# Optimization experiments

Measured on AMD Instinct MI355X. Metric: run time of the kernel, lower is better.

## Reference

```python
import jax, jax.numpy as jnp
import numpy as np

N = 100000
E = 1600000
C_IN = 128
C_OUT = 128


def setup_inputs() -> dict:
    key = jax.random.key(0)
    k1, k2, k3 = jax.random.split(key, 3)
    x = jax.random.normal(k1, (N, C_IN), dtype=jnp.float32)
    edge_index = jax.random.randint(k2, (2, E), 0, N, dtype=jnp.int64)
    # Linear(in, out, bias=False).weight has shape [out, in]
    W = jax.random.normal(k3, (C_OUT, C_IN), dtype=jnp.float32) * (1.0 / np.sqrt(C_IN))
    return {"x": x, "edge_index": edge_index, "W": W}


def reference(x, edge_index, W):
    n_nodes = x.shape[0]
    row, col = edge_index[0], edge_index[1]
    # degree counts only out-edges of row (matches torch `degree(edge_index, N)`)
    deg = jax.ops.segment_sum(jnp.ones((row.shape[0],), dtype=x.dtype), row,
                              num_segments=n_nodes)
    # D_tilde = D + I  ->  normalization n = (deg + 1)^(-1/2)
    inv_sqrt = jax.lax.rsqrt(deg + 1.0)  # [N]
    xs = x * inv_sqrt[:, None]
    # x <- (A + I) x : gather sources (col), scatter-add to destinations (row),
    # plus identity (self) contribution
    agg = jax.ops.segment_sum(xs[col], row, num_segments=n_nodes) + xs
    out = agg * inv_sqrt[:, None]
    # x <- x W^T
    return jnp.matmul(out, W.T)
```

## Files before the change

kernel.cpp:

```cpp
#include <hip/hip_runtime.h>
#include <hip/hip_fp16.h>
#include <math.h>

#define C 128
#define BSHIFT 9
#define BWIDTH 512
#define NBMAX 256
#define COLBITS 17
#define P2CHUNK 4096
#define P3CAP 10240
#define CAP 9216
#define APITCH 136

typedef _Float16 v8hf __attribute__((ext_vector_type(8)));
typedef float v4f __attribute__((ext_vector_type(4)));

__global__ __launch_bounds__(256) void init_wconv_kernel(int* __restrict__ gcur, int NB,
                                                         const float4* __restrict__ W4,
                                                         __half2* __restrict__ Wh2,
                                                         int total4) {
    int t = threadIdx.x;
    if (blockIdx.x == 0) {
        if (t < NB) gcur[t] = t * CAP;
    } else {
        int i = (blockIdx.x - 1) * 256 + t;
        if (i < total4) {
            float4 v = W4[i];
            Wh2[i * 2]     = __floats2half2_rn(v.x, v.y);
            Wh2[i * 2 + 1] = __floats2half2_rn(v.z, v.w);
        }
    }
}

__global__ __launch_bounds__(256) void p2_scatter_kernel(const int* __restrict__ rowI,
                                                         const int* __restrict__ colI,
                                                         int* __restrict__ gcur,
                                                         unsigned* __restrict__ ebuf, int E) {
    __shared__ int cnt[NBMAX];
    __shared__ int sc[NBMAX];
    __shared__ int delta[NBMAX];
    __shared__ unsigned sorted[P2CHUNK];
    __shared__ unsigned char bkt[P2CHUNK];
    const int t = threadIdx.x;
    cnt[t] = 0;
    __syncthreads();
    const int e0 = blockIdx.x * P2CHUNK;
    int ranks[16];
#pragma unroll
    for (int k = 0; k < 16; ++k) {
        int e = e0 + k * 256 + t;
        if (e < E) ranks[k] = atomicAdd(&cnt[rowI[e] >> BSHIFT], 1);
    }
    __syncthreads();
    sc[t] = cnt[t];
    __syncthreads();
    for (int o = 1; o < 256; o <<= 1) {
        int v = (t >= o) ? sc[t - o] : 0;
        __syncthreads();
        sc[t] += v;
        __syncthreads();
    }
    {
        int c = cnt[t];
        int ls = sc[t] - c;
        int gb = c ? atomicAdd(&gcur[t], c) : 0;
        delta[t] = gb - ls;
        sc[t] = ls;
    }
    __syncthreads();
#pragma unroll
    for (int k = 0; k < 16; ++k) {
        int e = e0 + k * 256 + t;
        if (e < E) {
            int r = rowI[e];
            unsigned cc = (unsigned)colI[e];
            int b = r >> BSHIFT;
            int lp = sc[b] + ranks[k];
            sorted[lp] = ((unsigned)(r & (BWIDTH - 1)) << COLBITS) | cc;
            bkt[lp] = (unsigned char)b;
        }
    }
    __syncthreads();
    int total = E - e0; if (total > P2CHUNK) total = P2CHUNK;
#pragma unroll
    for (int k = 0; k < 16; ++k) {
        int i = k * 256 + t;
        if (i < total) ebuf[delta[bkt[i]] + i] = sorted[i];
    }
}

__global__ __launch_bounds__(512) void p3_place_kernel(const unsigned* __restrict__ ebuf,
                                                       const int* __restrict__ gcur,
                                                       int* __restrict__ offs_start,
                                                       int* __restrict__ offs_end,
                                                       float* __restrict__ inv,
                                                       int* __restrict__ csr,
                                                       const float4* __restrict__ x4,
                                                       __half2* __restrict__ xsh2, int N) {
    __shared__ int cnt[BWIDTH];
    __shared__ int sc[BWIDTH];
    __shared__ float invS[BWIDTH];
    __shared__ int sortedCol[P3CAP];
    const int b = blockIdx.x;
    const int t = threadIdx.x;
    const int rowBase = b << BSHIFT;
    const int eS = b * CAP;
    const int eE = gcur[b];

    cnt[t] = 0;
    __syncthreads();
    for (int j = eS + t; j < eE; j += 512)
        atomicAdd(&cnt[ebuf[j] >> COLBITS], 1);
    __syncthreads();
    sc[t] = cnt[t];
    __syncthreads();
    for (int o = 1; o < 512; o <<= 1) {
        int v = (t >= o) ? sc[t - o] : 0;
        __syncthreads();
        sc[t] += v;
        __syncthreads();
    }
    int node = rowBase + t;
    int myCnt = cnt[t];
    float iv = rsqrtf((float)myCnt + 1.0f);
    invS[t] = iv;
    if (node < N) {
        offs_start[node] = eS + sc[t] - myCnt;
        offs_end[node]   = eS + sc[t];
        inv[node] = iv;
    }
    __syncthreads();
    cnt[t] = sc[t] - myCnt;
    __syncthreads();
    for (int j = eS + t; j < eE; j += 512) {
        unsigned rc = ebuf[j];
        int slot = atomicAdd(&cnt[rc >> COLBITS], 1);
        int col = (int)(rc & ((1u << COLBITS) - 1));
        if (slot < P3CAP) sortedCol[slot] = col;
        else csr[eS + slot] = col;
    }
    __syncthreads();
    int total = eE - eS; if (total > P3CAP) total = P3CAP;
    for (int i = t; i < total; i += 512)
        csr[eS + i] = sortedCol[i];

    int rows = N - rowBase; if (rows > BWIDTH) rows = BWIDTH;
    int limit = rows * 32;
    const float4* xr = x4 + (size_t)rowBase * 32;
    __half2* xd = xsh2 + (size_t)rowBase * 64;
    for (int i = t; i < limit; i += 512) {
        int row = i >> 5, ch = i & 31;
        float sI = invS[row];
        float4 v = xr[(size_t)row * 32 + ch];
        xd[(size_t)row * 64 + ch * 2]     = __floats2half2_rn(v.x * sI, v.y * sI);
        xd[(size_t)row * 64 + ch * 2 + 1] = __floats2half2_rn(v.z * sI, v.w * sI);
    }
}

#define ACC4(vv)                                                   \
    {                                                              \
        const __half2* p_ = (const __half2*)&(vv);                 \
        _Pragma("unroll")                                          \
        for (int q = 0; q < 4; ++q) {                              \
            float2 f_ = __half22float2(p_[q]);                     \
            a[2 * q] += f_.x; a[2 * q + 1] += f_.y;                \
        }                                                          \
    }

__global__ __launch_bounds__(256) void gather_mm_kernel(const float4* __restrict__ xsh4,
                                                        const int* __restrict__ offs_start,
                                                        const int* __restrict__ offs_end,
                                                        const int* __restrict__ csr,
                                                        const float* __restrict__ inv,
                                                        const _Float16* __restrict__ Wh,
                                                        float* __restrict__ out, int N) {
    __shared__ _Float16 agg[16][APITCH];
    const int tid = threadIdx.x;
    const int base = blockIdx.x * 16;
    const int r = tid >> 4;
    const int c16 = tid & 15;
    const int node = base + r;

    float a[8] = {0, 0, 0, 0, 0, 0, 0, 0};
    if (node < N) {
        int s = offs_start[node];
        int e = offs_end[node];
        {
            float4 h = xsh4[(size_t)node * 16 + c16];
            const __half2* p = (const __half2*)&h;
#pragma unroll
            for (int q = 0; q < 4; ++q) {
                float2 f = __half22float2(p[q]);
                a[2 * q] = f.x; a[2 * q + 1] = f.y;
            }
        }
        int j = s;
        for (; j + 4 <= e; j += 4) {
            int c0 = csr[j], c1 = csr[j + 1], c2 = csr[j + 2], c3 = csr[j + 3];
            float4 v0 = xsh4[(size_t)c0 * 16 + c16];
            float4 v1 = xsh4[(size_t)c1 * 16 + c16];
            float4 v2 = xsh4[(size_t)c2 * 16 + c16];
            float4 v3 = xsh4[(size_t)c3 * 16 + c16];
            ACC4(v0) ACC4(v1) ACC4(v2) ACC4(v3)
        }
        for (; j < e; ++j) {
            int c = csr[j];
            float4 v = xsh4[(size_t)c * 16 + c16];
            ACC4(v)
        }
        float invn = inv[node];
#pragma unroll
        for (int q = 0; q < 8; ++q) a[q] *= invn;
    }
    {
        __half2 hh[4];
#pragma unroll
        for (int q = 0; q < 4; ++q) hh[q] = __floats2half2_rn(a[2 * q], a[2 * q + 1]);
        *(float4*)&agg[r][c16 * 8] = *(const float4*)hh;
    }
    __syncthreads();

    const int wave = tid >> 6;
    const int lane = tid & 63;
    const int rr = lane & 15;
    const int kg = lane >> 4;

    v8hf av[4];
#pragma unroll
    for (int kk = 0; kk < 4; ++kk)
        av[kk] = *(const v8hf*)&agg[rr][kg * 8 + kk * 32];

#pragma unroll
    for (int ti = 0; ti < 2; ++ti) {
        const int t = wave * 2 + ti;
        v4f acc = {0.0f, 0.0f, 0.0f, 0.0f};
        const v8hf* bp = (const v8hf*)(Wh + (size_t)(t * 16 + rr) * C + kg * 8);
#pragma unroll
        for (int kk = 0; kk < 4; ++kk)
            acc = __builtin_amdgcn_mfma_f32_16x16x32_f16(av[kk], bp[kk * 4], acc, 0, 0, 0);
#pragma unroll
        for (int reg = 0; reg < 4; ++reg) {
            int orow = base + kg * 4 + reg;
            if (orow < N) out[(size_t)orow * C + t * 16 + rr] = acc[reg];
        }
    }
}

extern "C" void kernel_launch(void* const* d_in, const int* in_sizes, int n_in,
                              void* d_out, int out_size, void* d_ws, size_t ws_size,
                              hipStream_t stream) {
    const float* x  = (const float*)d_in[0];
    const int*   ei = (const int*)d_in[1];
    const float* W  = (const float*)d_in[2];
    float* out = (float*)d_out;

    const int N = in_sizes[0] / C;
    const int E = in_sizes[1] / 2;
    const int* rowI = ei;
    const int* colI = ei + E;

    const int NB = (N + BWIDTH - 1) / BWIDTH;

    char* ws = (char*)d_ws;
    size_t off = 0;
    auto carve = [&](size_t bytes) -> void* {
        off = (off + 255) & ~(size_t)255;
        void* p = ws + off;
        off += bytes;
        return p;
    };
    int*      gcur       = (int*)carve((size_t)NBMAX * 4);
    int*      offs_start = (int*)carve((size_t)N * 4);
    int*      offs_end   = (int*)carve((size_t)N * 4);
    float*    inv        = (float*)carve((size_t)N * 4);
    int*      csr        = (int*)carve((size_t)NB * CAP * 4);
    __half2*  xsh        = (__half2*)carve((size_t)N * C * 2);
    unsigned* ebuf       = (unsigned*)carve((size_t)NB * CAP * 4);
    __half2*  Wh         = (__half2*)carve((size_t)C * C * 2);

    int wtotal4 = C * C / 4;
    init_wconv_kernel<<<1 + (wtotal4 + 255) / 256, 256, 0, stream>>>(
        gcur, NB, (const float4*)W, Wh, wtotal4);

    int nChunks = (E + P2CHUNK - 1) / P2CHUNK;
    p2_scatter_kernel<<<nChunks, 256, 0, stream>>>(rowI, colI, gcur, ebuf, E);
    p3_place_kernel<<<NB, 512, 0, stream>>>(ebuf, gcur, offs_start, offs_end, inv, csr,
                                            (const float4*)x, xsh, N);

    gather_mm_kernel<<<(N + 15) / 16, 256, 0, stream>>>((const float4*)xsh, offs_start,
                                                        offs_end, csr, inv,
                                                        (const _Float16*)Wh, out, N);
}
```

Baseline: 131.7 us.

## Move fp16 conversion of x into scatter kernel and apply source norm in gather

The fp32-to-fp16 conversion of x moves from the place kernel, which runs on only about 196 blocks, into the scatter kernel, which has many more blocks, so the conversion gets more parallelism. Because the degree is not yet known at that point, the source normalisation moves into the gather loop. There it becomes an extra per-edge load of inv[col] folded in with an FMA. The cost is an additional random 4-byte gather per edge in the gather kernel.

```diff
diff --git a/kernel.cpp b/kernel.cpp
--- a/kernel.cpp
+++ b/kernel.cpp
@@ -35,7 +35,9 @@
 __global__ __launch_bounds__(256) void p2_scatter_kernel(const int* __restrict__ rowI,
                                                          const int* __restrict__ colI,
                                                          int* __restrict__ gcur,
-                                                         unsigned* __restrict__ ebuf, int E) {
+                                                         unsigned* __restrict__ ebuf, int E,
+                                                         const float4* __restrict__ x4,
+                                                         __half2* __restrict__ xh2, int N) {
     __shared__ int cnt[NBMAX];
     __shared__ int sc[NBMAX];
     __shared__ int delta[NBMAX];
@@ -87,6 +89,13 @@
         int i = k * 256 + t;
         if (i < total) ebuf[delta[bkt[i]] + i] = sorted[i];
     }
+
+    int totalX4 = N * 32;
+    for (int i = blockIdx.x * 256 + t; i < totalX4; i += gridDim.x * 256) {
+        float4 v = x4[i];
+        xh2[i * 2]     = __floats2half2_rn(v.x, v.y);
+        xh2[i * 2 + 1] = __floats2half2_rn(v.z, v.w);
+    }
 }
 
 __global__ __launch_bounds__(512) void p3_place_kernel(const unsigned* __restrict__ ebuf,
@@ -94,12 +103,9 @@
                                                        int* __restrict__ offs_start,
                                                        int* __restrict__ offs_end,
                                                        float* __restrict__ inv,
-                                                       int* __restrict__ csr,
-                                                       const float4* __restrict__ x4,
-                                                       __half2* __restrict__ xsh2, int N) {
+                                                       int* __restrict__ csr, int N) {
     __shared__ int cnt[BWIDTH];
     __shared__ int sc[BWIDTH];
-    __shared__ float invS[BWIDTH];
     __shared__ int sortedCol[P3CAP];
     const int b = blockIdx.x;
     const int t = threadIdx.x;
@@ -122,12 +128,10 @@
     }
     int node = rowBase + t;
     int myCnt = cnt[t];
-    float iv = rsqrtf((float)myCnt + 1.0f);
-    invS[t] = iv;
     if (node < N) {
         offs_start[node] = eS + sc[t] - myCnt;
         offs_end[node]   = eS + sc[t];
-        inv[node] = iv;
+        inv[node] = rsqrtf((float)myCnt + 1.0f);
     }
     __syncthreads();
     cnt[t] = sc[t] - myCnt;
@@ -143,31 +147,20 @@
     int total = eE - eS; if (total > P3CAP) total = P3CAP;
     for (int i = t; i < total; i += 512)
         csr[eS + i] = sortedCol[i];
-
-    int rows = N - rowBase; if (rows > BWIDTH) rows = BWIDTH;
-    int limit = rows * 32;
-    const float4* xr = x4 + (size_t)rowBase * 32;
-    __half2* xd = xsh2 + (size_t)rowBase * 64;
-    for (int i = t; i < limit; i += 512) {
-        int row = i >> 5, ch = i & 31;
-        float sI = invS[row];
-        float4 v = xr[(size_t)row * 32 + ch];
-        xd[(size_t)row * 64 + ch * 2]     = __floats2half2_rn(v.x * sI, v.y * sI);
-        xd[(size_t)row * 64 + ch * 2 + 1] = __floats2half2_rn(v.z * sI, v.w * sI);
-    }
-}
-
-#define ACC4(vv)                                                   \
+}
+
+#define ACC4F(vv, sI)                                              \
     {                                                              \
         const __half2* p_ = (const __half2*)&(vv);                 \
         _Pragma("unroll")                                          \
         for (int q = 0; q < 4; ++q) {                              \
             float2 f_ = __half22float2(p_[q]);                     \
-            a[2 * q] += f_.x; a[2 * q + 1] += f_.y;                \
+            a[2 * q]     = fmaf(f_.x, (sI), a[2 * q]);             \
+            a[2 * q + 1] = fmaf(f_.y, (sI), a[2 * q + 1]);         \
         }                                                          \
     }
 
-__global__ __launch_bounds__(256) void gather_mm_kernel(const float4* __restrict__ xsh4,
+__global__ __launch_bounds__(256) void gather_mm_kernel(const float4* __restrict__ xh4,
                                                         const int* __restrict__ offs_start,
                                                         const int* __restrict__ offs_end,
                                                         const int* __restrict__ csr,
@@ -182,33 +175,31 @@
     const int node = base + r;
 
     float a[8] = {0, 0, 0, 0, 0, 0, 0, 0};
+    float invn = 0.0f;
     if (node < N) {
         int s = offs_start[node];
         int e = offs_end[node];
+        invn = inv[node];
         {
-            float4 h = xsh4[(size_t)node * 16 + c16];
-            const __half2* p = (const __half2*)&h;
-#pragma unroll
-            for (int q = 0; q < 4; ++q) {
-                float2 f = __half22float2(p[q]);
-                a[2 * q] = f.x; a[2 * q + 1] = f.y;
-            }
+            float4 h = xh4[(size_t)node * 16 + c16];
+            ACC4F(h, invn)
         }
         int j = s;
         for (; j + 4 <= e; j += 4) {
             int c0 = csr[j], c1 = csr[j + 1], c2 = csr[j + 2], c3 = csr[j + 3];
-            float4 v0 = xsh4[(size_t)c0 * 16 + c16];
-            float4 v1 = xsh4[(size_t)c1 * 16 + c16];
-            float4 v2 = xsh4[(size_t)c2 * 16 + c16];
-            float4 v3 = xsh4[(size_t)c3 * 16 + c16];
-            ACC4(v0) ACC4(v1) ACC4(v2) ACC4(v3)
+            float i0 = inv[c0], i1 = inv[c1], i2 = inv[c2], i3 = inv[c3];
+            float4 v0 = xh4[(size_t)c0 * 16 + c16];
+            float4 v1 = xh4[(size_t)c1 * 16 + c16];
+            float4 v2 = xh4[(size_t)c2 * 16 + c16];
+            float4 v3 = xh4[(size_t)c3 * 16 + c16];
+            ACC4F(v0, i0) ACC4F(v1, i1) ACC4F(v2, i2) ACC4F(v3, i3)
         }
         for (; j < e; ++j) {
             int c = csr[j];
-            float4 v = xsh4[(size_t)c * 16 + c16];
-            ACC4(v)
-        }
-        float invn = inv[node];
+            float ic = inv[c];
+            float4 v = xh4[(size_t)c * 16 + c16];
+            ACC4F(v, ic)
+        }
 #pragma unroll
         for (int q = 0; q < 8; ++q) a[q] *= invn;
     }
@@ -274,7 +265,7 @@
     int*      offs_end   = (int*)carve((size_t)N * 4);
     float*    inv        = (float*)carve((size_t)N * 4);
     int*      csr        = (int*)carve((size_t)NB * CAP * 4);
-    __half2*  xsh        = (__half2*)carve((size_t)N * C * 2);
+    __half2*  xh         = (__half2*)carve((size_t)N * C * 2);
     unsigned* ebuf       = (unsigned*)carve((size_t)NB * CAP * 4);
     __half2*  Wh         = (__half2*)carve((size_t)C * C * 2);
 
@@ -283,11 +274,11 @@
         gcur, NB, (const float4*)W, Wh, wtotal4);
 
     int nChunks = (E + P2CHUNK - 1) / P2CHUNK;
-    p2_scatter_kernel<<<nChunks, 256, 0, stream>>>(rowI, colI, gcur, ebuf, E);
-    p3_place_kernel<<<NB, 512, 0, stream>>>(ebuf, gcur, offs_start, offs_end, inv, csr,
-                                            (const float4*)x, xsh, N);
-
-    gather_mm_kernel<<<(N + 15) / 16, 256, 0, stream>>>((const float4*)xsh, offs_start,
+    p2_scatter_kernel<<<nChunks, 256, 0, stream>>>(rowI, colI, gcur, ebuf, E,
+                                                   (const float4*)x, xh, N);
+    p3_place_kernel<<<NB, 512, 0, stream>>>(ebuf, gcur, offs_start, offs_end, inv, csr, N);
+
+    gather_mm_kernel<<<(N + 15) / 16, 256, 0, stream>>>((const float4*)xh, offs_start,
                                                         offs_end, csr, inv,
                                                         (const _Float16*)Wh, out, N);
 }
```

Result: no change. 129.3 us (-1.8%).
